# Kernel tuning notes

Measured on AMD Instinct MI355X. Metric: run time of the kernel, lower is better.

Reference implementation:

```python
import jax, jax.numpy as jnp
import numpy as np

N_USERS = 2213
N_SOURCES = 50000
D = 128
H = 8
BATCH = 1024


def setup_inputs() -> dict:
    key = jax.random.key(0)
    k1, k2, k3, k4, k5, k6 = jax.random.split(key, 6)
    X_user_id = jax.random.randint(k1, (BATCH,), 0, N_USERS)
    user_emb = jax.random.normal(k2, (N_USERS, D), dtype=jnp.float32)
    source_emb = jax.random.normal(k3, (N_SOURCES, D), dtype=jnp.float32)
    Wcm = jax.random.normal(k4, (H, D, D), dtype=jnp.float32) * 0.05
    W1 = jax.random.normal(k5, (H * D, D), dtype=jnp.float32) * 0.05
    A_us = jax.random.uniform(k6, (N_USERS, N_SOURCES), dtype=jnp.float32)
    return {"X_user_id": X_user_id, "user_emb": user_emb, "source_emb": source_emb,
            "Wcm": Wcm, "W1": W1, "A_us": A_us}


def reference(X_user_id, user_emb, source_emb, Wcm, W1, A_us):
    d = user_emb.shape[-1]
    scale = jnp.sqrt(jnp.asarray(d, dtype=user_emb.dtype))
    Xu = user_emb[X_user_id]            # [b, d]
    A = A_us[X_user_id]                 # [b, S] dense adjacency rows
    M = source_emb                      # [S, d]
    n_heads = Wcm.shape[0]
    m_hat = []
    for i in range(n_heads):            # small fixed head loop (keeps [b,S] peak memory per head)
        scores = jnp.einsum('bd,de,se->bs', Xu, Wcm[i], M) / scale
        scores = jax.nn.relu(scores)
        alpha = jax.nn.softmax(scores * A, axis=-1)   # dropout is identity in eval
        m_hat.append(alpha @ M)         # [b, d]
    m = jnp.concatenate(m_hat, axis=-1) @ W1          # [b, d]
    user_rep = jax.nn.elu(m) + Xu
    return user_rep
```

## Files before the change

### kernel.cpp

```cpp
#include <hip/hip_runtime.h>
#include <hip/hip_bf16.h>
#include <math.h>


#define S_TOT 50000
#define S_PAD 50304
#define DDIM 128
#define NHEAD 8
#define NB 1024
#define BQ 32
#define SN 32
#define NCH 8
#define SCHUNK 6272
#define NBT 32

typedef __bf16 v8bf __attribute__((ext_vector_type(8)));
typedef float v4f __attribute__((ext_vector_type(4)));

union U4BF { uint4 u; v8bf b; };

__device__ inline unsigned short f2bf(float f) {
  union { float f; unsigned u; } v; v.f = f;
  unsigned r = (v.u + 0x7FFFu + ((v.u >> 16) & 1u)) >> 16;
  return (unsigned short)r;
}

__global__ void k_qproj(const int* __restrict__ uid, const float* __restrict__ user_emb,
                        const float* __restrict__ Wcm, unsigned short* __restrict__ Qbf) {
  int bh = blockIdx.x;
  int b = bh >> 3, h = bh & 7;
  int e = threadIdx.x;
  int u = uid[b];
  const float* xu = user_emb + (long)u * DDIM;
  const float* w = Wcm + (long)h * DDIM * DDIM + e;
  float acc = 0.f;
#pragma unroll 16
  for (int d = 0; d < DDIM; ++d) acc += xu[d] * w[(long)d * DDIM];
  Qbf[(long)bh * DDIM + e] = f2bf(acc * 0.08838834764831845f);
}

__global__ void k_convM(const float* __restrict__ M, unsigned short* __restrict__ Mbf) {
  long i = (long)(blockIdx.x * 256 + threadIdx.x) * 8;
  if (i >= (long)S_PAD * DDIM) return;
  union { unsigned short s[8]; uint4 u; } o;
  if (i < (long)S_TOT * DDIM) {
    const float4* p = (const float4*)(M + i);
    float4 a = p[0], b = p[1];
    o.s[0] = f2bf(a.x); o.s[1] = f2bf(a.y); o.s[2] = f2bf(a.z); o.s[3] = f2bf(a.w);
    o.s[4] = f2bf(b.x); o.s[5] = f2bf(b.y); o.s[6] = f2bf(b.z); o.s[7] = f2bf(b.w);
  } else {
    o.u.x = 0; o.u.y = 0; o.u.z = 0; o.u.w = 0;
  }
  *(uint4*)(Mbf + i) = o.u;
}

__global__ void k_transM(const unsigned short* __restrict__ Mbf, unsigned short* __restrict__ MbfT) {
  __shared__ unsigned short tile[64][65];
  int s0 = blockIdx.x * 64, d0 = blockIdx.y * 64;
  int t = threadIdx.x;
#pragma unroll
  for (int it = 0; it < 16; ++it) {
    int flat = t + 256 * it;
    int sl = flat >> 6, dl = flat & 63;
    tile[sl][dl] = Mbf[(long)(s0 + sl) * DDIM + d0 + dl];
  }
  __syncthreads();
#pragma unroll
  for (int it = 0; it < 16; ++it) {
    int flat = t + 256 * it;
    int dl = flat >> 6, sl = flat & 63;
    MbfT[(long)(d0 + dl) * S_PAD + s0 + sl] = tile[sl][dl];
  }
}

__launch_bounds__(512, 2)
__global__ void k_attn(const int* __restrict__ uid_g, const float* __restrict__ A_us,
                       const unsigned short* __restrict__ Qbf,
                       const unsigned short* __restrict__ Mbf,
                       const unsigned short* __restrict__ MbfT,
                       float* __restrict__ part_acc, float* __restrict__ part_sum) {
  __shared__ __align__(16) unsigned short lds_M[SN][136];
  __shared__ __align__(16) unsigned short lds_Mt[DDIM][40];
  __shared__ __align__(16) unsigned short lds_P[256][40];
  __shared__ __align__(16) float lds_At[SN][36];
  __shared__ int lds_uid[BQ];

  int ch = blockIdx.x;
  int bt = blockIdx.y;
  int tid = threadIdx.x;
  int w = tid >> 6;
  int lane = tid & 63;
  int q = lane >> 4, li = lane & 15;

  if (tid < BQ) lds_uid[tid] = uid_g[bt * BQ + tid];

  U4BF qf[2][4];
#pragma unroll
  for (int mt = 0; mt < 2; ++mt)
#pragma unroll
    for (int k = 0; k < 4; ++k) {
      int b = bt * BQ + mt * 16 + li;
      qf[mt][k].u = *(const uint4*)(Qbf + ((long)(b * NHEAD + w) * DDIM + k * 32 + q * 8));
    }

  v4f zero4 = {0.f, 0.f, 0.f, 0.f};
  v4f acc[2][8];
#pragma unroll
  for (int mt = 0; mt < 2; ++mt)
#pragma unroll
    for (int dt = 0; dt < 8; ++dt) acc[mt][dt] = zero4;
  float sE[2][4] = {{0.f,0.f,0.f,0.f},{0.f,0.f,0.f,0.f}};

  __syncthreads();

  int s_beg = ch * SCHUNK;
  int s_fin = s_beg + SCHUNK;
  if (s_fin > S_TOT) s_fin = S_TOT;

  for (int s0 = s_beg; s0 < s_fin; s0 += SN) {
    {
      int sl = tid >> 4, d = (tid & 15) * 8;
      uint4 mv = *(const uint4*)(Mbf + (long)(s0 + sl) * DDIM + d);
      *(uint4*)&lds_M[sl][d] = mv;

      int dd2 = tid >> 2, pp = (tid & 3) * 8;
      uint4 tv = *(const uint4*)(MbfT + (long)dd2 * S_PAD + s0 + pp);
      *(uint4*)&lds_Mt[dd2][pp] = tv;

      if (tid < 256) {
        int bl = tid >> 3, sq = (tid & 7) * 4;
        const float* arow = A_us + (long)lds_uid[bl] * S_TOT;
        int sg = s0 + sq;
        float4 av;
        if (sg + 3 < S_TOT) {
          av = *(const float4*)(arow + sg);
        } else {
          av.x = (sg + 0 < S_TOT) ? arow[sg + 0] : 0.f;
          av.y = (sg + 1 < S_TOT) ? arow[sg + 1] : 0.f;
          av.z = (sg + 2 < S_TOT) ? arow[sg + 2] : 0.f;
          av.w = (sg + 3 < S_TOT) ? arow[sg + 3] : 0.f;
        }
        lds_At[sq + 0][bl] = av.x;
        lds_At[sq + 1][bl] = av.y;
        lds_At[sq + 2][bl] = av.z;
        lds_At[sq + 3][bl] = av.w;
      }
    }
    __syncthreads();

    U4BF bfm[2][4];
#pragma unroll
    for (int nt = 0; nt < 2; ++nt)
#pragma unroll
      for (int k = 0; k < 4; ++k)
        bfm[nt][k].u = *(const uint4*)&lds_M[nt * 16 + li][k * 32 + q * 8];

    v4f c[2][2];
    c[0][0] = zero4; c[0][1] = zero4; c[1][0] = zero4; c[1][1] = zero4;
#pragma unroll
    for (int k = 0; k < 4; ++k)
#pragma unroll
      for (int mt = 0; mt < 2; ++mt)
#pragma unroll
        for (int nt = 0; nt < 2; ++nt)
          c[mt][nt] = __builtin_amdgcn_mfma_f32_16x16x32_bf16(qf[mt][k].b, bfm[nt][k].b, c[mt][nt], 0, 0, 0);

#pragma unroll
    for (int mt = 0; mt < 2; ++mt)
#pragma unroll
      for (int nt = 0; nt < 2; ++nt) {
        int sloc = nt * 16 + li;
        float vmask = ((s0 + sloc) < S_TOT) ? 1.f : 0.f;
        const float4 a4 = *(const float4*)&lds_At[sloc][mt * 16 + q * 4];
        float aarr[4] = {a4.x, a4.y, a4.z, a4.w};
#pragma unroll
        for (int r = 0; r < 4; ++r) {
          float sc = fmaxf(c[mt][nt][r], 0.f) * aarr[r];
          float p = __expf(sc) * vmask;
          sE[mt][r] += p;
          lds_P[w * 32 + mt * 16 + q * 4 + r][sloc] = f2bf(p);
        }
      }
    __syncthreads();

    U4BF pf[2];
#pragma unroll
    for (int mt = 0; mt < 2; ++mt)
      pf[mt].u = *(const uint4*)&lds_P[w * 32 + mt * 16 + li][q * 8];
#pragma unroll
    for (int dt = 0; dt < 8; ++dt) {
      U4BF mf;
      mf.u = *(const uint4*)&lds_Mt[dt * 16 + li][q * 8];
#pragma unroll
      for (int mt = 0; mt < 2; ++mt)
        acc[mt][dt] = __builtin_amdgcn_mfma_f32_16x16x32_bf16(pf[mt].b, mf.b, acc[mt][dt], 0, 0, 0);
    }
    __syncthreads();
  }

  long base = ((long)ch * NBT + bt) * 256;
#pragma unroll
  for (int mt = 0; mt < 2; ++mt)
#pragma unroll
    for (int dt = 0; dt < 8; ++dt)
#pragma unroll
      for (int r = 0; r < 4; ++r) {
        int m = w * 32 + mt * 16 + q * 4 + r;
        part_acc[(base + m) * DDIM + dt * 16 + li] = acc[mt][dt][r];
      }
#pragma unroll
  for (int mt = 0; mt < 2; ++mt)
#pragma unroll
    for (int r = 0; r < 4; ++r) {
      float v = sE[mt][r];
      v += __shfl_xor(v, 1);
      v += __shfl_xor(v, 2);
      v += __shfl_xor(v, 4);
      v += __shfl_xor(v, 8);
      if (li == 0) part_sum[base + w * 32 + mt * 16 + q * 4 + r] = v;
    }
}

__global__ void k_reduce(const float* __restrict__ part_acc, const float* __restrict__ part_sum,
                         float* __restrict__ hhat) {
  int g = blockIdx.x * 256 + threadIdx.x;
  int bt = g >> 15;
  int m = (g >> 7) & 255;
  int e = g & 127;
  float a = 0.f, s = 0.f;
#pragma unroll
  for (int ch = 0; ch < NCH; ++ch) {
    long base = ((long)ch * NBT + bt) * 256 + m;
    a += part_acc[base * DDIM + e];
    s += part_sum[base];
  }
  int h = m >> 5, bl = m & 31;
  int b = bt * BQ + bl;
  hhat[(long)b * 1024 + h * DDIM + e] = a / s;
}

__global__ void k_final(const float* __restrict__ hhat, const float* __restrict__ W1,
                        const int* __restrict__ uid, const float* __restrict__ user_emb,
                        float* __restrict__ out) {
  int blk = blockIdx.x;
  int d = threadIdx.x & 127;
  int half = threadIdx.x >> 7;
  int b0 = blk * 16 + half * 8;
  float acc[8] = {0.f,0.f,0.f,0.f,0.f,0.f,0.f,0.f};
  for (int k = 0; k < 1024; ++k) {
    float wv = W1[(long)k * DDIM + d];
#pragma unroll
    for (int j = 0; j < 8; ++j) acc[j] += hhat[(long)(b0 + j) * 1024 + k] * wv;
  }
#pragma unroll
  for (int j = 0; j < 8; ++j) {
    int b = b0 + j;
    float x = acc[j];
    float e = (x > 0.f) ? x : expm1f(x);
    out[(long)b * DDIM + d] = e + user_emb[(long)uid[b] * DDIM + d];
  }
}

extern "C" void kernel_launch(void* const* d_in, const int* in_sizes, int n_in,
                              void* d_out, int out_size, void* d_ws, size_t ws_size,
                              hipStream_t stream) {
  const int* uid        = (const int*)d_in[0];
  const float* user_emb = (const float*)d_in[1];
  const float* src_emb  = (const float*)d_in[2];
  const float* Wcm      = (const float*)d_in[3];
  const float* W1       = (const float*)d_in[4];
  const float* A_us     = (const float*)d_in[5];
  float* out = (float*)d_out;

  char* ws = (char*)d_ws;
  unsigned short* Qbf  = (unsigned short*)(ws + 0);
  unsigned short* Mbf  = (unsigned short*)(ws + 2097152);
  unsigned short* MbfT = (unsigned short*)(ws + 14974976);
  float* part_acc      = (float*)(ws + 27852800);
  float* part_sum      = (float*)(ws + 61407232);
  float* hhat          = (float*)(ws + 61669376);

  k_qproj<<<dim3(NB * NHEAD), dim3(128), 0, stream>>>(uid, user_emb, Wcm, Qbf);
  k_convM<<<dim3((S_PAD * DDIM / 8 + 255) / 256), dim3(256), 0, stream>>>(src_emb, Mbf);
  k_transM<<<dim3(S_PAD / 64, DDIM / 64), dim3(256), 0, stream>>>(Mbf, MbfT);
  k_attn<<<dim3(NCH, NBT), dim3(512), 0, stream>>>(uid, A_us, Qbf, Mbf, MbfT, part_acc, part_sum);
  k_reduce<<<dim3(NBT * 256 * DDIM / 256), dim3(256), 0, stream>>>(part_acc, part_sum, hhat);
  k_final<<<dim3(64), dim3(256), 0, stream>>>(hhat, W1, uid, user_emb, out);
}
```

Before: 1.091 ms.

## Double-buffer attention staging, fuse M prep, split S finer, shrink partials

Fuses the bf16 conversion and transpose of source embeddings into one kernel. In the attention kernel it doubles the source-chunk count, double-buffers LDS staging so the next tile loads while the current one computes, and raises the occupancy hint. It drops the per-element padding mask and instead subtracts a constant pad count from the softmax denominator. It also truncates probabilities to bf16 rather than rounding, stores partial accumulators as bf16, and spreads the final projection over more blocks. These steps cut memory traffic and raise parallelism at some cost in precision.

```diff
diff --git a/kernel.cpp b/kernel.cpp
--- a/kernel.cpp
+++ b/kernel.cpp
@@ -10,9 +10,11 @@
 #define NB 1024
 #define BQ 32
 #define SN 32
-#define NCH 8
-#define SCHUNK 6272
+#define NCH 16
+#define SCHUNK 3136
+#define NIT (SCHUNK / SN)
 #define NBT 32
+#define PAD_CNT 176.0f
 
 typedef __bf16 v8bf __attribute__((ext_vector_type(8)));
 typedef float v4f __attribute__((ext_vector_type(4)));
@@ -39,30 +41,20 @@
   Qbf[(long)bh * DDIM + e] = f2bf(acc * 0.08838834764831845f);
 }
 
-__global__ void k_convM(const float* __restrict__ M, unsigned short* __restrict__ Mbf) {
-  long i = (long)(blockIdx.x * 256 + threadIdx.x) * 8;
-  if (i >= (long)S_PAD * DDIM) return;
-  union { unsigned short s[8]; uint4 u; } o;
-  if (i < (long)S_TOT * DDIM) {
-    const float4* p = (const float4*)(M + i);
-    float4 a = p[0], b = p[1];
-    o.s[0] = f2bf(a.x); o.s[1] = f2bf(a.y); o.s[2] = f2bf(a.z); o.s[3] = f2bf(a.w);
-    o.s[4] = f2bf(b.x); o.s[5] = f2bf(b.y); o.s[6] = f2bf(b.z); o.s[7] = f2bf(b.w);
-  } else {
-    o.u.x = 0; o.u.y = 0; o.u.z = 0; o.u.w = 0;
-  }
-  *(uint4*)(Mbf + i) = o.u;
-}
-
-__global__ void k_transM(const unsigned short* __restrict__ Mbf, unsigned short* __restrict__ MbfT) {
-  __shared__ unsigned short tile[64][65];
+__global__ void k_prepM(const float* __restrict__ M, unsigned short* __restrict__ Mbf,
+                        unsigned short* __restrict__ MbfT) {
+  __shared__ unsigned short tile[64][66];
   int s0 = blockIdx.x * 64, d0 = blockIdx.y * 64;
   int t = threadIdx.x;
 #pragma unroll
   for (int it = 0; it < 16; ++it) {
     int flat = t + 256 * it;
     int sl = flat >> 6, dl = flat & 63;
-    tile[sl][dl] = Mbf[(long)(s0 + sl) * DDIM + d0 + dl];
+    int s = s0 + sl;
+    float v = (s < S_TOT) ? M[(long)s * DDIM + d0 + dl] : 0.f;
+    unsigned short bb = f2bf(v);
+    tile[sl][dl] = bb;
+    Mbf[(long)s * DDIM + d0 + dl] = bb;
   }
   __syncthreads();
 #pragma unroll
@@ -73,24 +65,24 @@
   }
 }
 
-__launch_bounds__(512, 2)
+__launch_bounds__(512, 4)
 __global__ void k_attn(const int* __restrict__ uid_g, const float* __restrict__ A_us,
                        const unsigned short* __restrict__ Qbf,
                        const unsigned short* __restrict__ Mbf,
                        const unsigned short* __restrict__ MbfT,
-                       float* __restrict__ part_acc, float* __restrict__ part_sum) {
-  __shared__ __align__(16) unsigned short lds_M[SN][136];
-  __shared__ __align__(16) unsigned short lds_Mt[DDIM][40];
+                       unsigned short* __restrict__ part_acc, float* __restrict__ part_sum) {
+  __shared__ __align__(16) unsigned short lds_M[2][SN][136];
+  __shared__ __align__(16) unsigned short lds_Mt[2][DDIM][40];
   __shared__ __align__(16) unsigned short lds_P[256][40];
-  __shared__ __align__(16) float lds_At[SN][36];
+  __shared__ __align__(16) float lds_At[2][SN][36];
   __shared__ int lds_uid[BQ];
 
-  int ch = blockIdx.x;
-  int bt = blockIdx.y;
-  int tid = threadIdx.x;
-  int w = tid >> 6;
-  int lane = tid & 63;
-  int q = lane >> 4, li = lane & 15;
+  const int ch = blockIdx.x;
+  const int bt = blockIdx.y;
+  const int tid = threadIdx.x;
+  const int w = tid >> 6;
+  const int lane = tid & 63;
+  const int q = lane >> 4, li = lane & 15;
 
   if (tid < BQ) lds_uid[tid] = uid_g[bt * BQ + tid];
 
@@ -113,47 +105,47 @@
 
   __syncthreads();
 
-  int s_beg = ch * SCHUNK;
-  int s_fin = s_beg + SCHUNK;
-  if (s_fin > S_TOT) s_fin = S_TOT;
-
-  for (int s0 = s_beg; s0 < s_fin; s0 += SN) {
-    {
-      int sl = tid >> 4, d = (tid & 15) * 8;
-      uint4 mv = *(const uint4*)(Mbf + (long)(s0 + sl) * DDIM + d);
-      *(uint4*)&lds_M[sl][d] = mv;
-
-      int dd2 = tid >> 2, pp = (tid & 3) * 8;
-      uint4 tv = *(const uint4*)(MbfT + (long)dd2 * S_PAD + s0 + pp);
-      *(uint4*)&lds_Mt[dd2][pp] = tv;
-
-      if (tid < 256) {
-        int bl = tid >> 3, sq = (tid & 7) * 4;
-        const float* arow = A_us + (long)lds_uid[bl] * S_TOT;
-        int sg = s0 + sq;
-        float4 av;
-        if (sg + 3 < S_TOT) {
-          av = *(const float4*)(arow + sg);
-        } else {
-          av.x = (sg + 0 < S_TOT) ? arow[sg + 0] : 0.f;
-          av.y = (sg + 1 < S_TOT) ? arow[sg + 1] : 0.f;
-          av.z = (sg + 2 < S_TOT) ? arow[sg + 2] : 0.f;
-          av.w = (sg + 3 < S_TOT) ? arow[sg + 3] : 0.f;
-        }
-        lds_At[sq + 0][bl] = av.x;
-        lds_At[sq + 1][bl] = av.y;
-        lds_At[sq + 2][bl] = av.z;
-        lds_At[sq + 3][bl] = av.w;
+  const int s_beg = ch * SCHUNK;
+
+  auto stage = [&](int buf, int s0) {
+    int sl = tid >> 4, d = (tid & 15) * 8;
+    *(uint4*)&lds_M[buf][sl][d] = *(const uint4*)(Mbf + (long)(s0 + sl) * DDIM + d);
+    int dd = tid >> 2, pp = (tid & 3) * 8;
+    *(uint4*)&lds_Mt[buf][dd][pp] = *(const uint4*)(MbfT + (long)dd * S_PAD + s0 + pp);
+    if (tid < 256) {
+      int bl = tid >> 3, sq = (tid & 7) * 4;
+      const float* arow = A_us + (long)lds_uid[bl] * S_TOT;
+      int sg = s0 + sq;
+      float4 av;
+      if (sg + 3 < S_TOT) {
+        av = *(const float4*)(arow + sg);
+      } else {
+        av.x = (sg + 0 < S_TOT) ? arow[sg + 0] : 0.f;
+        av.y = (sg + 1 < S_TOT) ? arow[sg + 1] : 0.f;
+        av.z = (sg + 2 < S_TOT) ? arow[sg + 2] : 0.f;
+        av.w = (sg + 3 < S_TOT) ? arow[sg + 3] : 0.f;
       }
-    }
-    __syncthreads();
+      lds_At[buf][sq + 0][bl] = av.x;
+      lds_At[buf][sq + 1][bl] = av.y;
+      lds_At[buf][sq + 2][bl] = av.z;
+      lds_At[buf][sq + 3][bl] = av.w;
+    }
+  };
+
+  stage(0, s_beg);
+  __syncthreads();
+
+  for (int it = 0; it < NIT; ++it) {
+    const int p = it & 1;
+    const int s0 = s_beg + it * SN;
+    if (it + 1 < NIT) stage(1 - p, s0 + SN);
 
     U4BF bfm[2][4];
 #pragma unroll
     for (int nt = 0; nt < 2; ++nt)
 #pragma unroll
       for (int k = 0; k < 4; ++k)
-        bfm[nt][k].u = *(const uint4*)&lds_M[nt * 16 + li][k * 32 + q * 8];
+        bfm[nt][k].u = *(const uint4*)&lds_M[p][nt * 16 + li][k * 32 + q * 8];
 
     v4f c[2][2];
     c[0][0] = zero4; c[0][1] = zero4; c[1][0] = zero4; c[1][1] = zero4;
@@ -170,15 +162,15 @@
 #pragma unroll
       for (int nt = 0; nt < 2; ++nt) {
         int sloc = nt * 16 + li;
-        float vmask = ((s0 + sloc) < S_TOT) ? 1.f : 0.f;
-        const float4 a4 = *(const float4*)&lds_At[sloc][mt * 16 + q * 4];
+        const float4 a4 = *(const float4*)&lds_At[p][sloc][mt * 16 + q * 4];
         float aarr[4] = {a4.x, a4.y, a4.z, a4.w};
 #pragma unroll
         for (int r = 0; r < 4; ++r) {
           float sc = fmaxf(c[mt][nt][r], 0.f) * aarr[r];
-          float p = __expf(sc) * vmask;
-          sE[mt][r] += p;
-          lds_P[w * 32 + mt * 16 + q * 4 + r][sloc] = f2bf(p);
+          float pv = __expf(sc);
+          sE[mt][r] += pv;
+          lds_P[w * 32 + mt * 16 + q * 4 + r][sloc] =
+              (unsigned short)(__float_as_uint(pv) >> 16);
         }
       }
     __syncthreads();
@@ -190,7 +182,7 @@
 #pragma unroll
     for (int dt = 0; dt < 8; ++dt) {
       U4BF mf;
-      mf.u = *(const uint4*)&lds_Mt[dt * 16 + li][q * 8];
+      mf.u = *(const uint4*)&lds_Mt[p][dt * 16 + li][q * 8];
 #pragma unroll
       for (int mt = 0; mt < 2; ++mt)
         acc[mt][dt] = __builtin_amdgcn_mfma_f32_16x16x32_bf16(pf[mt].b, mf.b, acc[mt][dt], 0, 0, 0);
@@ -206,7 +198,7 @@
 #pragma unroll
       for (int r = 0; r < 4; ++r) {
         int m = w * 32 + mt * 16 + q * 4 + r;
-        part_acc[(base + m) * DDIM + dt * 16 + li] = acc[mt][dt][r];
+        part_acc[(base + m) * DDIM + dt * 16 + li] = f2bf(acc[mt][dt][r]);
       }
 #pragma unroll
   for (int mt = 0; mt < 2; ++mt)
@@ -221,8 +213,8 @@
     }
 }
 
-__global__ void k_reduce(const float* __restrict__ part_acc, const float* __restrict__ part_sum,
-                         float* __restrict__ hhat) {
+__global__ void k_reduce(const unsigned short* __restrict__ part_acc,
+                         const float* __restrict__ part_sum, float* __restrict__ hhat) {
   int g = blockIdx.x * 256 + threadIdx.x;
   int bt = g >> 15;
   int m = (g >> 7) & 255;
@@ -231,9 +223,11 @@
 #pragma unroll
   for (int ch = 0; ch < NCH; ++ch) {
     long base = ((long)ch * NBT + bt) * 256 + m;
-    a += part_acc[base * DDIM + e];
+    unsigned ub = part_acc[base * DDIM + e];
+    a += __uint_as_float(ub << 16);
     s += part_sum[base];
   }
+  s -= PAD_CNT;
   int h = m >> 5, bl = m & 31;
   int b = bt * BQ + bl;
   hhat[(long)b * 1024 + h * DDIM + e] = a / s;
@@ -245,20 +239,20 @@
   int blk = blockIdx.x;
   int d = threadIdx.x & 127;
   int half = threadIdx.x >> 7;
-  int b0 = blk * 16 + half * 8;
-  float acc[8] = {0.f,0.f,0.f,0.f,0.f,0.f,0.f,0.f};
+  int b0 = blk * 4 + half * 2;
+  float a0 = 0.f, a1 = 0.f;
+  const float* h0 = hhat + (long)b0 * 1024;
+  const float* h1 = h0 + 1024;
+#pragma unroll 8
   for (int k = 0; k < 1024; ++k) {
     float wv = W1[(long)k * DDIM + d];
-#pragma unroll
-    for (int j = 0; j < 8; ++j) acc[j] += hhat[(long)(b0 + j) * 1024 + k] * wv;
-  }
-#pragma unroll
-  for (int j = 0; j < 8; ++j) {
-    int b = b0 + j;
-    float x = acc[j];
-    float e = (x > 0.f) ? x : expm1f(x);
-    out[(long)b * DDIM + d] = e + user_emb[(long)uid[b] * DDIM + d];
-  }
+    a0 += h0[k] * wv;
+    a1 += h1[k] * wv;
+  }
+  float e0 = (a0 > 0.f) ? a0 : expm1f(a0);
+  float e1 = (a1 > 0.f) ? a1 : expm1f(a1);
+  out[(long)b0 * DDIM + d]         = e0 + user_emb[(long)uid[b0] * DDIM + d];
+  out[(long)(b0 + 1) * DDIM + d]   = e1 + user_emb[(long)uid[b0 + 1] * DDIM + d];
 }
 
 extern "C" void kernel_launch(void* const* d_in, const int* in_sizes, int n_in,
@@ -273,17 +267,16 @@
   float* out = (float*)d_out;
 
   char* ws = (char*)d_ws;
-  unsigned short* Qbf  = (unsigned short*)(ws + 0);
-  unsigned short* Mbf  = (unsigned short*)(ws + 2097152);
-  unsigned short* MbfT = (unsigned short*)(ws + 14974976);
-  float* part_acc      = (float*)(ws + 27852800);
-  float* part_sum      = (float*)(ws + 61407232);
-  float* hhat          = (float*)(ws + 61669376);
+  unsigned short* Qbf      = (unsigned short*)(ws + 0);
+  unsigned short* Mbf      = (unsigned short*)(ws + 2097152);
+  unsigned short* MbfT     = (unsigned short*)(ws + 14974976);
+  unsigned short* part_acc = (unsigned short*)(ws + 27852800);
+  float* part_sum          = (float*)(ws + 61407232);
+  float* hhat              = (float*)(ws + 61931520);
 
   k_qproj<<<dim3(NB * NHEAD), dim3(128), 0, stream>>>(uid, user_emb, Wcm, Qbf);
-  k_convM<<<dim3((S_PAD * DDIM / 8 + 255) / 256), dim3(256), 0, stream>>>(src_emb, Mbf);
-  k_transM<<<dim3(S_PAD / 64, DDIM / 64), dim3(256), 0, stream>>>(Mbf, MbfT);
+  k_prepM<<<dim3(S_PAD / 64, DDIM / 64), dim3(256), 0, stream>>>(src_emb, Mbf, MbfT);
   k_attn<<<dim3(NCH, NBT), dim3(512), 0, stream>>>(uid, A_us, Qbf, Mbf, MbfT, part_acc, part_sum);
   k_reduce<<<dim3(NBT * 256 * DDIM / 256), dim3(256), 0, stream>>>(part_acc, part_sum, hhat);
-  k_final<<<dim3(64), dim3(256), 0, stream>>>(hhat, W1, uid, user_emb, out);
-}
+  k_final<<<dim3(256), dim3(256), 0, stream>>>(hhat, W1, uid, user_emb, out);
+}
```

Result: no change. 1.078 ms (-1.3%).
